# Kernel tuning notes

Hardware: AMD Instinct MI355X
Metric: run time of the kernel (lower is better)

## Reference

```python
import jax, jax.numpy as jnp
import numpy as np

B = 65536          # number of graphs
NPG = 28           # nodes per graph (896 = 32*28)
N = B * NPG
K = 4              # random within-graph neighbors per node


def setup_inputs() -> dict:
    key = jax.random.key(0)
    ks = jax.random.split(key, 8)
    x = jax.random.normal(ks[0], (N, 2), dtype=jnp.float32)
    # within-graph random edges: each node i -> K random targets in its graph
    local = jax.random.randint(ks[1], (N, K), 0, NPG)
    base = (jnp.arange(N, dtype=jnp.int32) // NPG) * NPG
    dst = (base[:, None] + local.astype(jnp.int32)).reshape(-1)
    src = jnp.repeat(jnp.arange(N, dtype=jnp.int32), K)
    edge_index = jnp.stack([src, dst])  # [2, E]
    conv_w = jax.random.normal(ks[2], (2, 32), dtype=jnp.float32) * (1.0 / np.sqrt(2))
    conv_b = jax.random.normal(ks[3], (32,), dtype=jnp.float32) * 0.01
    fc1_w = jax.random.normal(ks[4], (896, 256), dtype=jnp.float32) * (1.0 / np.sqrt(896))
    fc1_b = jax.random.normal(ks[5], (256,), dtype=jnp.float32) * 0.01
    fc2_w = jax.random.normal(ks[6], (256, 2), dtype=jnp.float32) * (1.0 / np.sqrt(256))
    fc2_b = jax.random.normal(ks[7], (2,), dtype=jnp.float32) * 0.01
    return {"x": x, "edge_index": edge_index, "conv_w": conv_w, "conv_b": conv_b,
            "fc1_w": fc1_w, "fc1_b": fc1_b, "fc2_w": fc2_w, "fc2_b": fc2_b}


def gcn_conv(x, edge_index, w, b):
    n = x.shape[0]
    h = x @ w  # [N, 32]
    loops = jnp.arange(n, dtype=edge_index.dtype)
    src = jnp.concatenate([edge_index[0], loops])
    dst = jnp.concatenate([edge_index[1], loops])
    deg = jax.ops.segment_sum(jnp.ones_like(dst, dtype=h.dtype), dst, num_segments=n)
    dinv = jnp.where(deg > 0, jax.lax.rsqrt(jnp.maximum(deg, 1.0)), 0.0)
    norm = dinv[src] * dinv[dst]  # [E']
    agg = jax.ops.segment_sum(h[src] * norm[:, None], dst, num_segments=n)
    return agg + b


def reference(x, edge_index, conv_w, conv_b, fc1_w, fc1_b, fc2_w, fc2_b):
    h = jax.nn.relu(gcn_conv(x, edge_index, conv_w, conv_b))  # [N, 32]
    h = h.reshape(-1, 896)                                    # [B, 896]
    h = h @ fc1_w + fc1_b                                     # [B, 256]
    nrm = jnp.sqrt(jnp.sum(h * h, axis=1, keepdims=True))
    hn = h / jnp.maximum(nrm, 1e-12)                          # F.normalize(dim=1)
    x1 = hn @ fc2_w + fc2_b                                   # [B, 2]
    mu = jax.nn.sigmoid(x1[:, 0])
    theta = jax.nn.softplus(x1[:, 1])
    return hn, mu, theta
```

## Files before the change

### kernel.cpp

```cpp
#include <hip/hip_runtime.h>
#include <hip/hip_bf16.h>
#include <stdint.h>

#define NPG 28
#define KDIM 896
#define NOUT 256
#define BM 128
#define BK 32
#define KT (KDIM / BK)

typedef __attribute__((ext_vector_type(8))) __bf16 bf16x8;
typedef __attribute__((ext_vector_type(8))) ushort us8;
typedef __attribute__((ext_vector_type(4))) float f32x4;

__device__ __forceinline__ ushort f2bf(float v) {
    uint u = __float_as_uint(v);
    return (ushort)((u + 0x7fffu + ((u >> 16) & 1u)) >> 16);
}

__device__ __forceinline__ void gload_lds16(const void* g, void* l) {
    __builtin_amdgcn_global_load_lds(
        (const __attribute__((address_space(1))) void*)(uintptr_t)g,
        (__attribute__((address_space(3))) void*)(uintptr_t)l,
        16, 0, 0);
}

__global__ __launch_bounds__(256) void k_agg(
    const float* __restrict__ x, const int* __restrict__ dst,
    const float* __restrict__ f1w,
    float* __restrict__ acc2g, ushort* __restrict__ wt, int nAgg)
{
    __shared__ int   pk[8][32];
    __shared__ float sx[8][32][2];
    __shared__ float t[32][33];

    const int tid = threadIdx.x;

    if ((int)blockIdx.x >= nAgg) {
        int b = blockIdx.x - nAgg;
        int n0 = (b & 7) * 32, k0 = (b >> 3) * 32;
        int tx = tid & 31, ty = tid >> 5;
#pragma unroll
        for (int q = 0; q < 4; ++q)
            t[ty + q * 8][tx] = f1w[(k0 + ty + q * 8) * NOUT + n0 + tx];
        __syncthreads();
#pragma unroll
        for (int q = 0; q < 4; ++q)
            wt[(long)(k0 >> 5) * (NOUT * BK) + (n0 + ty + q * 8) * BK + tx] =
                f2bf(t[tx][ty + q * 8]);
        return;
    }

    const int g = tid >> 5;
    const int j = tid & 31;
    const long gb = ((long)blockIdx.x * 8 + g) * NPG;

    float2 xx = make_float2(0.f, 0.f);
    if (j < NPG) {
        int4 d4 = ((const int4*)dst)[gb + j];
        xx = ((const float2*)x)[gb + j];
        int gbi = (int)gb;
        pk[g][j] = (d4.x - gbi) | ((d4.y - gbi) << 8) |
                   ((d4.z - gbi) << 16) | ((d4.w - gbi) << 24);
    }
    __syncthreads();

    const uint repj = (uint)j * 0x01010101u;
    uint cp0 = 0, cp1 = 0, cp2 = 0, cp3 = 0;
    int cnt = 0;
#pragma unroll
    for (int s4 = 0; s4 < 7; ++s4) {
        int4 pv = *(const int4*)&pk[g][s4 * 4];
#pragma unroll
        for (int r = 0; r < 4; ++r) {
            uint v = ((const uint*)&pv)[r] ^ repj;
            uint zb = ~(((v & 0x7F7F7F7Fu) + 0x7F7F7F7Fu) | v) & 0x80808080u;
            uint c = (uint)__popc(zb);
            cnt += (int)c;
            int s = s4 * 4 + r;
            uint nib = c << ((s & 7) * 4);
            if (s < 8)       cp0 |= nib;
            else if (s < 16) cp1 |= nib;
            else if (s < 24) cp2 |= nib;
            else             cp3 |= nib;
        }
    }

    const float dinv = rsqrtf((float)(1 + cnt));
    const float sx0 = xx.x * dinv, sx1 = xx.y * dinv;
    if (j < NPG) {
        sx[g][j][0] = sx0;
        sx[g][j][1] = sx1;
    }
    __syncthreads();

    float a0 = sx0, a1 = sx1;
#pragma unroll
    for (int s = 0; s < NPG; ++s) {
        float2 sv = *(const float2*)&sx[g][s][0];
        uint cpw = (s < 8) ? cp0 : (s < 16) ? cp1 : (s < 24) ? cp2 : cp3;
        float cf = (float)((cpw >> ((s & 7) * 4)) & 0xFu);
        a0 += cf * sv.x;
        a1 += cf * sv.y;
    }

    if (j < NPG) {
        const long Btot = (long)nAgg * 8;
        const long graph = (long)blockIdx.x * 8 + g;
        ((float2*)acc2g)[(long)j * Btot + graph] = make_float2(a0 * dinv, a1 * dinv);
    }
}

__device__ __forceinline__ void stage_b2(const char* WtB, ushort* BsX, int kt, int tid) {
    const int o = (tid & 3) ^ ((tid >> 3) & 3);
    const long tb = (long)kt * 16384 + (tid >> 2) * 64 + o * 16;
    gload_lds16(WtB + tb,        (char*)BsX + tid * 16);
    gload_lds16(WtB + tb + 8192, (char*)BsX + 8192 + tid * 16);
}

__device__ __forceinline__ void agen_write(ushort* AsX, float2 av, int awoff,
                                           const float* w0, const float* w1, const float* bb) {
    union { us8 v; uint u[4]; } pk;
#pragma unroll
    for (int k = 0; k < 4; ++k) {
        float e0 = fmaxf(av.x * w0[2 * k]     + av.y * w1[2 * k]     + bb[2 * k],     0.f);
        float e1 = fmaxf(av.x * w0[2 * k + 1] + av.y * w1[2 * k + 1] + bb[2 * k + 1], 0.f);
        __hip_bfloat162 h = __float22bfloat162_rn(make_float2(e0, e1));
        pk.u[k] = *reinterpret_cast<uint*>(&h);
    }
    *(us8*)&AsX[awoff] = pk.v;
}

__device__ __forceinline__ void compute_mfma(const ushort* AsX, const ushort* BsX,
                                             f32x4 acc[4][4], int a_off, int b_off) {
    bf16x8 bfr[4];
#pragma unroll
    for (int ni = 0; ni < 4; ++ni)
        bfr[ni] = *(const bf16x8*)(&BsX[b_off + ni * 512]);
    __builtin_amdgcn_s_setprio(1);
#pragma unroll
    for (int mi = 0; mi < 4; ++mi) {
        bf16x8 af = *(const bf16x8*)(&AsX[a_off + mi * 512]);
#pragma unroll
        for (int ni = 0; ni < 4; ++ni)
            acc[mi][ni] = __builtin_amdgcn_mfma_f32_16x16x32_bf16(
                af, bfr[ni], acc[mi][ni], 0, 0, 0);
    }
    __builtin_amdgcn_s_setprio(0);
}

__global__ __launch_bounds__(512, 4) void k_gemm(
    const float* __restrict__ acc2g, const ushort* __restrict__ Wt,
    const float* __restrict__ cw, const float* __restrict__ cb,
    const float* __restrict__ f1b, const float* __restrict__ f2w,
    const float* __restrict__ f2b, float* __restrict__ out, int Bsz)
{
    __shared__ ushort As0[BM * BK], As1[BM * BK];
    __shared__ ushort Bs0[NOUT * BK], Bs1[NOUT * BK], Bs2[NOUT * BK];
    __shared__ float2 Aring[2][8][64];

    const int tid = threadIdx.x;
    const int w = tid >> 6, l = tid & 63;
    const int wM = w >> 2, wN = w & 3;
    const int l15 = l & 15, lhi = (l >> 4) & 3;
    const long m0 = (long)blockIdx.x * BM;
    const long BszB = (long)Bsz * 8;

    const int ao = __builtin_amdgcn_readfirstlane(w & 3);
    const int arow = (w >> 2) * 64 + l;
    const int awoff = arow * 32 + ((ao ^ ((l >> 1) & 3)) * 8);
    float w0[8], w1[8], bb[8];
#pragma unroll
    for (int k = 0; k < 8; ++k) {
        w0[k] = cw[ao * 8 + k]; w1[k] = cw[32 + ao * 8 + k]; bb[k] = cb[ao * 8 + k];
    }

    const int swz = (lhi ^ ((l15 >> 1) & 3)) * 8;
    const int a_off = (wM * 64 + l15) * 32 + swz;
    const int b_off = (wN * 64 + l15) * 32 + swz;

    const char* A2B = (const char*)acc2g;
    const char* WtB = (const char*)Wt;
    const long agbase = (m0 + (long)(w >> 2) * 64 + 2 * l) * 8;

    f32x4 acc[4][4];
#pragma unroll
    for (int mi = 0; mi < 4; ++mi)
#pragma unroll
        for (int ni = 0; ni < 4; ++ni) acc[mi][ni] = (f32x4){0.f, 0.f, 0.f, 0.f};

    stage_b2(WtB, Bs0, 0, tid);
    if (l < 32) gload_lds16(A2B + agbase,        (char*)&Aring[0][w][0]);
    stage_b2(WtB, Bs1, 1, tid);
    if (l < 32) gload_lds16(A2B + BszB + agbase, (char*)&Aring[1][w][0]);
    asm volatile("s_waitcnt vmcnt(3)" ::: "memory");
    __builtin_amdgcn_s_barrier();
    agen_write(As0, Aring[0][w][l], awoff, w0, w1, bb);
    asm volatile("s_waitcnt lgkmcnt(0)" ::: "memory");
    __builtin_amdgcn_s_barrier();

#define PH(BC, BS, AC, AN, RR, RS, KS) do {                                    \
        stage_b2(WtB, BS, (KS), tid);                                          \
        if (l < 32) gload_lds16(A2B + (long)(KS) * BszB + agbase,              \
                                (char*)&Aring[RS][w][0]);                      \
        compute_mfma(AC, BC, acc, a_off, b_off);                               \
        asm volatile("s_waitcnt vmcnt(3)" ::: "memory");                       \
        agen_write(AN, Aring[RR][w][l], awoff, w0, w1, bb);                    \
        asm volatile("s_waitcnt lgkmcnt(0)" ::: "memory");                     \
        __builtin_amdgcn_s_barrier();                                          \
    } while (0)

    for (int kt = 0; kt < 24; kt += 6) {
        PH(Bs0, Bs2, As0, As1, 1, 0, kt + 2);
        PH(Bs1, Bs0, As1, As0, 0, 1, kt + 3);
        PH(Bs2, Bs1, As0, As1, 1, 0, kt + 4);
        PH(Bs0, Bs2, As1, As0, 0, 1, kt + 5);
        PH(Bs1, Bs0, As0, As1, 1, 0, kt + 6);
        PH(Bs2, Bs1, As1, As0, 0, 1, kt + 7);
    }
    PH(Bs0, Bs2, As0, As1, 1, 0, 26);
    PH(Bs1, Bs0, As1, As0, 0, 1, 27);
    {
        compute_mfma(As0, Bs2, acc, a_off, b_off);
        asm volatile("s_waitcnt vmcnt(0)" ::: "memory");
        agen_write(As1, Aring[1][w][l], awoff, w0, w1, bb);
        asm volatile("s_waitcnt lgkmcnt(0)" ::: "memory");
        __builtin_amdgcn_s_barrier();
    }
    {
        compute_mfma(As1, Bs0, acc, a_off, b_off);
        asm volatile("s_waitcnt lgkmcnt(0)" ::: "memory");
        __builtin_amdgcn_s_barrier();
    }
#undef PH

    float b1[4], w20[4], w21[4];
#pragma unroll
    for (int ni = 0; ni < 4; ++ni) {
        int col = wN * 64 + ni * 16 + l15;
        b1[ni] = f1b[col];
        w20[ni] = f2w[col * 2 + 0];
        w21[ni] = f2w[col * 2 + 1];
    }
    float* red    = (float*)As0;
    float* red_ss = red;
    float* red_p0 = red + 512;
    float* red_p1 = red + 1024;
    float* red_rn = red + 1536;

#pragma unroll
    for (int mi = 0; mi < 4; ++mi) {
        float ssr[4], p0r[4], p1r[4];
#pragma unroll
        for (int r = 0; r < 4; ++r) { ssr[r] = 0.f; p0r[r] = 0.f; p1r[r] = 0.f; }
#pragma unroll
        for (int ni = 0; ni < 4; ++ni) {
#pragma unroll
            for (int r = 0; r < 4; ++r) {
                float v = acc[mi][ni][r] + b1[ni];
                acc[mi][ni][r] = v;
                ssr[r] += v * v;
                p0r[r] += v * w20[ni];
                p1r[r] += v * w21[ni];
            }
        }
#pragma unroll
        for (int m = 1; m < 16; m <<= 1) {
#pragma unroll
            for (int r = 0; r < 4; ++r) {
                ssr[r] += __shfl_xor(ssr[r], m);
                p0r[r] += __shfl_xor(p0r[r], m);
                p1r[r] += __shfl_xor(p1r[r], m);
            }
        }
        if (l15 == 0) {
            int rowb = wM * 64 + mi * 16 + lhi * 4;
#pragma unroll
            for (int r = 0; r < 4; ++r) {
                red_ss[(rowb + r) * 4 + wN] = ssr[r];
                red_p0[(rowb + r) * 4 + wN] = p0r[r];
                red_p1[(rowb + r) * 4 + wN] = p1r[r];
            }
        }
    }
    __syncthreads();

    if (tid < BM) {
        int row = tid;
        float ss = red_ss[row * 4 + 0] + red_ss[row * 4 + 1] + red_ss[row * 4 + 2] + red_ss[row * 4 + 3];
        float p0 = red_p0[row * 4 + 0] + red_p0[row * 4 + 1] + red_p0[row * 4 + 2] + red_p0[row * 4 + 3];
        float p1 = red_p1[row * 4 + 0] + red_p1[row * 4 + 1] + red_p1[row * 4 + 2] + red_p1[row * 4 + 3];
        float rn = 1.0f / fmaxf(sqrtf(ss), 1e-12f);
        float x0 = p0 * rn + f2b[0];
        float x1 = p1 * rn + f2b[1];
        float mu = 1.0f / (1.0f + expf(-x0));
        float th = (x1 > 0.f) ? (x1 + log1pf(expf(-x1))) : log1pf(expf(x1));
        long gr = m0 + row;
        out[(long)Bsz * NOUT + gr] = mu;
        out[(long)Bsz * NOUT + Bsz + gr] = th;
        red_rn[row] = rn;
    }
    __syncthreads();

#pragma unroll
    for (int mi = 0; mi < 4; ++mi) {
        float rn[4];
#pragma unroll
        for (int r = 0; r < 4; ++r) rn[r] = red_rn[wM * 64 + mi * 16 + lhi * 4 + r];
#pragma unroll
        for (int ni = 0; ni < 4; ++ni) {
#pragma unroll
            for (int r = 0; r < 4; ++r) {
                long row = m0 + wM * 64 + mi * 16 + lhi * 4 + r;
                out[row * NOUT + wN * 64 + ni * 16 + l15] = acc[mi][ni][r] * rn[r];
            }
        }
    }
}

extern "C" void kernel_launch(void* const* d_in, const int* in_sizes, int n_in,
                              void* d_out, int out_size, void* d_ws, size_t ws_size,
                              hipStream_t stream) {
    const float* x   = (const float*)d_in[0];
    const int*   ei  = (const int*)d_in[1];
    const float* cw  = (const float*)d_in[2];
    const float* cb  = (const float*)d_in[3];
    const float* f1w = (const float*)d_in[4];
    const float* f1b = (const float*)d_in[5];
    const float* f2w = (const float*)d_in[6];
    const float* f2b = (const float*)d_in[7];
    float* out = (float*)d_out;

    const int Nn  = in_sizes[0] / 2;
    const int Bsz = Nn / NPG;
    const int E   = in_sizes[1] / 2;
    const int* dst = ei + E;

    float*  acc2g = (float*)d_ws;
    ushort* Wt    = (ushort*)(acc2g + (size_t)Nn * 2);

    const int nAgg = Bsz / 8;
    const int nTr  = (KDIM / 32) * (NOUT / 32);

    k_agg<<<nAgg + nTr, 256, 0, stream>>>(x, dst, f1w, acc2g, Wt, nAgg);
    k_gemm<<<Bsz / BM, 512, 0, stream>>>(acc2g, Wt, cw, cb, f1b, f2w, f2b, out, Bsz);
}
```

Baseline: 66.92 us.

## Fuse graph aggregation into GEMM kernel and double M tile

Moves the per-graph degree/aggregation computation into the GEMM kernel, storing aggregated node features in LDS instead of a global workspace, and leaves a small weight-transpose prep kernel. BM grows to 256 with 1024-thread blocks, so each B stage is one load per thread. This removes the global write and readback of the aggregated features. In exchange it needs a large LDS footprint that limits residency to one block per CU, and the aggregation runs serially inside each block before the GEMM starts.

```diff
diff --git a/kernel.cpp b/kernel.cpp
--- a/kernel.cpp
+++ b/kernel.cpp
@@ -5,7 +5,7 @@
 #define NPG 28
 #define KDIM 896
 #define NOUT 256
-#define BM 128
+#define BM 256
 #define BK 32
 #define KT (KDIM / BK)
 
@@ -25,97 +25,28 @@
         16, 0, 0);
 }
 
-__global__ __launch_bounds__(256) void k_agg(
-    const float* __restrict__ x, const int* __restrict__ dst,
-    const float* __restrict__ f1w,
-    float* __restrict__ acc2g, ushort* __restrict__ wt, int nAgg)
+__global__ __launch_bounds__(256) void k_prep(const float* __restrict__ f1w,
+                                              ushort* __restrict__ wt)
 {
-    __shared__ int   pk[8][32];
-    __shared__ float sx[8][32][2];
     __shared__ float t[32][33];
-
     const int tid = threadIdx.x;
-
-    if ((int)blockIdx.x >= nAgg) {
-        int b = blockIdx.x - nAgg;
-        int n0 = (b & 7) * 32, k0 = (b >> 3) * 32;
-        int tx = tid & 31, ty = tid >> 5;
-#pragma unroll
-        for (int q = 0; q < 4; ++q)
-            t[ty + q * 8][tx] = f1w[(k0 + ty + q * 8) * NOUT + n0 + tx];
-        __syncthreads();
-#pragma unroll
-        for (int q = 0; q < 4; ++q)
-            wt[(long)(k0 >> 5) * (NOUT * BK) + (n0 + ty + q * 8) * BK + tx] =
-                f2bf(t[tx][ty + q * 8]);
-        return;
-    }
-
-    const int g = tid >> 5;
-    const int j = tid & 31;
-    const long gb = ((long)blockIdx.x * 8 + g) * NPG;
-
-    float2 xx = make_float2(0.f, 0.f);
-    if (j < NPG) {
-        int4 d4 = ((const int4*)dst)[gb + j];
-        xx = ((const float2*)x)[gb + j];
-        int gbi = (int)gb;
-        pk[g][j] = (d4.x - gbi) | ((d4.y - gbi) << 8) |
-                   ((d4.z - gbi) << 16) | ((d4.w - gbi) << 24);
-    }
+    int b = blockIdx.x;
+    int n0 = (b & 7) * 32, k0 = (b >> 3) * 32;
+    int tx = tid & 31, ty = tid >> 5;
+#pragma unroll
+    for (int q = 0; q < 4; ++q)
+        t[ty + q * 8][tx] = f1w[(k0 + ty + q * 8) * NOUT + n0 + tx];
     __syncthreads();
-
-    const uint repj = (uint)j * 0x01010101u;
-    uint cp0 = 0, cp1 = 0, cp2 = 0, cp3 = 0;
-    int cnt = 0;
-#pragma unroll
-    for (int s4 = 0; s4 < 7; ++s4) {
-        int4 pv = *(const int4*)&pk[g][s4 * 4];
-#pragma unroll
-        for (int r = 0; r < 4; ++r) {
-            uint v = ((const uint*)&pv)[r] ^ repj;
-            uint zb = ~(((v & 0x7F7F7F7Fu) + 0x7F7F7F7Fu) | v) & 0x80808080u;
-            uint c = (uint)__popc(zb);
-            cnt += (int)c;
-            int s = s4 * 4 + r;
-            uint nib = c << ((s & 7) * 4);
-            if (s < 8)       cp0 |= nib;
-            else if (s < 16) cp1 |= nib;
-            else if (s < 24) cp2 |= nib;
-            else             cp3 |= nib;
-        }
-    }
-
-    const float dinv = rsqrtf((float)(1 + cnt));
-    const float sx0 = xx.x * dinv, sx1 = xx.y * dinv;
-    if (j < NPG) {
-        sx[g][j][0] = sx0;
-        sx[g][j][1] = sx1;
-    }
-    __syncthreads();
-
-    float a0 = sx0, a1 = sx1;
-#pragma unroll
-    for (int s = 0; s < NPG; ++s) {
-        float2 sv = *(const float2*)&sx[g][s][0];
-        uint cpw = (s < 8) ? cp0 : (s < 16) ? cp1 : (s < 24) ? cp2 : cp3;
-        float cf = (float)((cpw >> ((s & 7) * 4)) & 0xFu);
-        a0 += cf * sv.x;
-        a1 += cf * sv.y;
-    }
-
-    if (j < NPG) {
-        const long Btot = (long)nAgg * 8;
-        const long graph = (long)blockIdx.x * 8 + g;
-        ((float2*)acc2g)[(long)j * Btot + graph] = make_float2(a0 * dinv, a1 * dinv);
-    }
-}
-
-__device__ __forceinline__ void stage_b2(const char* WtB, ushort* BsX, int kt, int tid) {
+#pragma unroll
+    for (int q = 0; q < 4; ++q)
+        wt[(long)(k0 >> 5) * (NOUT * BK) + (n0 + ty + q * 8) * BK + tx] =
+            f2bf(t[tx][ty + q * 8]);
+}
+
+__device__ __forceinline__ void stage_b1(const char* WtB, ushort* BsX, int kt, int tid) {
     const int o = (tid & 3) ^ ((tid >> 3) & 3);
-    const long tb = (long)kt * 16384 + (tid >> 2) * 64 + o * 16;
-    gload_lds16(WtB + tb,        (char*)BsX + tid * 16);
-    gload_lds16(WtB + tb + 8192, (char*)BsX + 8192 + tid * 16);
+    gload_lds16(WtB + (long)kt * 16384 + (tid >> 2) * 64 + o * 16,
+                (char*)BsX + tid * 16);
 }
 
 __device__ __forceinline__ void agen_write(ushort* AsX, float2 av, int awoff,
@@ -149,22 +80,101 @@
     __builtin_amdgcn_s_setprio(0);
 }
 
-__global__ __launch_bounds__(512, 4) void k_gemm(
-    const float* __restrict__ acc2g, const ushort* __restrict__ Wt,
+__global__ __launch_bounds__(1024, 4) void k_fused(
+    const float* __restrict__ x, const int* __restrict__ dst,
+    const ushort* __restrict__ Wt,
     const float* __restrict__ cw, const float* __restrict__ cb,
     const float* __restrict__ f1b, const float* __restrict__ f2w,
     const float* __restrict__ f2b, float* __restrict__ out, int Bsz)
 {
     __shared__ ushort As0[BM * BK], As1[BM * BK];
     __shared__ ushort Bs0[NOUT * BK], Bs1[NOUT * BK], Bs2[NOUT * BK];
-    __shared__ float2 Aring[2][8][64];
+    __shared__ float2 Agg[NPG][BM];
 
     const int tid = threadIdx.x;
     const int w = tid >> 6, l = tid & 63;
     const int wM = w >> 2, wN = w & 3;
     const int l15 = l & 15, lhi = (l >> 4) & 3;
     const long m0 = (long)blockIdx.x * BM;
-    const long BszB = (long)Bsz * 8;
+    const char* WtB = (const char*)Wt;
+
+    stage_b1(WtB, Bs0, 0, tid);
+    stage_b1(WtB, Bs1, 1, tid);
+
+    {
+        int*   pks = (int*)As0;
+        float* sxp = (float*)As1;
+        const int g5 = tid >> 5;
+        const int j  = tid & 31;
+
+        int4 d4 = make_int4(0, 0, 0, 0);
+        float2 xx = make_float2(0.f, 0.f);
+        {
+            long gb = (m0 + (long)g5 * 8) * NPG;
+            if (j < NPG) {
+                d4 = ((const int4*)dst)[gb + j];
+                xx = ((const float2*)x)[gb + j];
+            }
+        }
+        for (int it = 0; it < 8; ++it) {
+            const int gr = g5 * 8 + it;
+            const long gb = (m0 + gr) * NPG;
+            int4 d4n = make_int4(0, 0, 0, 0);
+            float2 xxn = make_float2(0.f, 0.f);
+            if (it < 7 && j < NPG) {
+                d4n = ((const int4*)dst)[gb + NPG + j];
+                xxn = ((const float2*)x)[gb + NPG + j];
+            }
+            if (j < NPG) {
+                int gbi = (int)gb;
+                pks[g5 * 32 + j] = (d4.x - gbi) | ((d4.y - gbi) << 8) |
+                                   ((d4.z - gbi) << 16) | ((d4.w - gbi) << 24);
+            }
+            asm volatile("s_waitcnt lgkmcnt(0)" ::: "memory");
+
+            const uint repj = (uint)j * 0x01010101u;
+            uint cp0 = 0, cp1 = 0, cp2 = 0, cp3 = 0;
+            int cnt = 0;
+#pragma unroll
+            for (int s4 = 0; s4 < 7; ++s4) {
+                int4 pv = *(const int4*)&pks[g5 * 32 + s4 * 4];
+#pragma unroll
+                for (int r = 0; r < 4; ++r) {
+                    uint v = ((const uint*)&pv)[r] ^ repj;
+                    uint zb = ~(((v & 0x7F7F7F7Fu) + 0x7F7F7F7Fu) | v) & 0x80808080u;
+                    uint c = (uint)__popc(zb);
+                    cnt += (int)c;
+                    int s = s4 * 4 + r;
+                    uint nib = c << ((s & 7) * 4);
+                    if (s < 8)       cp0 |= nib;
+                    else if (s < 16) cp1 |= nib;
+                    else if (s < 24) cp2 |= nib;
+                    else             cp3 |= nib;
+                }
+            }
+
+            const float dinv = rsqrtf((float)(1 + cnt));
+            const float sx0 = xx.x * dinv, sx1 = xx.y * dinv;
+            if (j < NPG) {
+                sxp[(g5 * 32 + j) * 2]     = sx0;
+                sxp[(g5 * 32 + j) * 2 + 1] = sx1;
+            }
+            asm volatile("s_waitcnt lgkmcnt(0)" ::: "memory");
+
+            float a0 = sx0, a1 = sx1;
+#pragma unroll
+            for (int s = 0; s < NPG; ++s) {
+                float2 sv = *(const float2*)&sxp[(g5 * 32 + s) * 2];
+                uint cpw = (s < 8) ? cp0 : (s < 16) ? cp1 : (s < 24) ? cp2 : cp3;
+                float cf = (float)((cpw >> ((s & 7) * 4)) & 0xFu);
+                a0 += cf * sv.x;
+                a1 += cf * sv.y;
+            }
+            if (j < NPG)
+                Agg[j][gr] = make_float2(a0 * dinv, a1 * dinv);
+            d4 = d4n; xx = xxn;
+        }
+    }
 
     const int ao = __builtin_amdgcn_readfirstlane(w & 3);
     const int arow = (w >> 2) * 64 + l;
@@ -174,56 +184,44 @@
     for (int k = 0; k < 8; ++k) {
         w0[k] = cw[ao * 8 + k]; w1[k] = cw[32 + ao * 8 + k]; bb[k] = cb[ao * 8 + k];
     }
-
     const int swz = (lhi ^ ((l15 >> 1) & 3)) * 8;
     const int a_off = (wM * 64 + l15) * 32 + swz;
     const int b_off = (wN * 64 + l15) * 32 + swz;
 
-    const char* A2B = (const char*)acc2g;
-    const char* WtB = (const char*)Wt;
-    const long agbase = (m0 + (long)(w >> 2) * 64 + 2 * l) * 8;
-
     f32x4 acc[4][4];
 #pragma unroll
     for (int mi = 0; mi < 4; ++mi)
 #pragma unroll
         for (int ni = 0; ni < 4; ++ni) acc[mi][ni] = (f32x4){0.f, 0.f, 0.f, 0.f};
 
-    stage_b2(WtB, Bs0, 0, tid);
-    if (l < 32) gload_lds16(A2B + agbase,        (char*)&Aring[0][w][0]);
-    stage_b2(WtB, Bs1, 1, tid);
-    if (l < 32) gload_lds16(A2B + BszB + agbase, (char*)&Aring[1][w][0]);
-    asm volatile("s_waitcnt vmcnt(3)" ::: "memory");
-    __builtin_amdgcn_s_barrier();
-    agen_write(As0, Aring[0][w][l], awoff, w0, w1, bb);
+    __syncthreads();
+    agen_write(As0, Agg[0][arow], awoff, w0, w1, bb);
     asm volatile("s_waitcnt lgkmcnt(0)" ::: "memory");
     __builtin_amdgcn_s_barrier();
 
-#define PH(BC, BS, AC, AN, RR, RS, KS) do {                                    \
-        stage_b2(WtB, BS, (KS), tid);                                          \
-        if (l < 32) gload_lds16(A2B + (long)(KS) * BszB + agbase,              \
-                                (char*)&Aring[RS][w][0]);                      \
+#define PH(BC, BS, AC, AN, KS) do {                                            \
+        stage_b1(WtB, BS, (KS), tid);                                          \
         compute_mfma(AC, BC, acc, a_off, b_off);                               \
-        asm volatile("s_waitcnt vmcnt(3)" ::: "memory");                       \
-        agen_write(AN, Aring[RR][w][l], awoff, w0, w1, bb);                    \
+        asm volatile("s_waitcnt vmcnt(1)" ::: "memory");                       \
+        agen_write(AN, Agg[(KS) - 1][arow], awoff, w0, w1, bb);                \
         asm volatile("s_waitcnt lgkmcnt(0)" ::: "memory");                     \
         __builtin_amdgcn_s_barrier();                                          \
     } while (0)
 
     for (int kt = 0; kt < 24; kt += 6) {
-        PH(Bs0, Bs2, As0, As1, 1, 0, kt + 2);
-        PH(Bs1, Bs0, As1, As0, 0, 1, kt + 3);
-        PH(Bs2, Bs1, As0, As1, 1, 0, kt + 4);
-        PH(Bs0, Bs2, As1, As0, 0, 1, kt + 5);
-        PH(Bs1, Bs0, As0, As1, 1, 0, kt + 6);
-        PH(Bs2, Bs1, As1, As0, 0, 1, kt + 7);
-    }
-    PH(Bs0, Bs2, As0, As1, 1, 0, 26);
-    PH(Bs1, Bs0, As1, As0, 0, 1, 27);
+        PH(Bs0, Bs2, As0, As1, kt + 2);
+        PH(Bs1, Bs0, As1, As0, kt + 3);
+        PH(Bs2, Bs1, As0, As1, kt + 4);
+        PH(Bs0, Bs2, As1, As0, kt + 5);
+        PH(Bs1, Bs0, As0, As1, kt + 6);
+        PH(Bs2, Bs1, As1, As0, kt + 7);
+    }
+    PH(Bs0, Bs2, As0, As1, 26);
+    PH(Bs1, Bs0, As1, As0, 27);
     {
         compute_mfma(As0, Bs2, acc, a_off, b_off);
         asm volatile("s_waitcnt vmcnt(0)" ::: "memory");
-        agen_write(As1, Aring[1][w][l], awoff, w0, w1, bb);
+        agen_write(As1, Agg[27][arow], awoff, w0, w1, bb);
         asm volatile("s_waitcnt lgkmcnt(0)" ::: "memory");
         __builtin_amdgcn_s_barrier();
     }
@@ -244,9 +242,9 @@
     }
     float* red    = (float*)As0;
     float* red_ss = red;
-    float* red_p0 = red + 512;
-    float* red_p1 = red + 1024;
-    float* red_rn = red + 1536;
+    float* red_p0 = red + 1024;
+    float* red_p1 = red + 2048;
+    float* red_rn = red + 3072;
 
 #pragma unroll
     for (int mi = 0; mi < 4; ++mi) {
@@ -336,12 +334,9 @@
     const int E   = in_sizes[1] / 2;
     const int* dst = ei + E;
 
-    float*  acc2g = (float*)d_ws;
-    ushort* Wt    = (ushort*)(acc2g + (size_t)Nn * 2);
-
-    const int nAgg = Bsz / 8;
-    const int nTr  = (KDIM / 32) * (NOUT / 32);
-
-    k_agg<<<nAgg + nTr, 256, 0, stream>>>(x, dst, f1w, acc2g, Wt, nAgg);
-    k_gemm<<<Bsz / BM, 512, 0, stream>>>(acc2g, Wt, cw, cb, f1b, f2w, f2b, out, Bsz);
-}
+    ushort* Wt = (ushort*)d_ws;
+
+    const int nTr = (KDIM / 32) * (NOUT / 32);
+    k_prep<<<nTr, 256, 0, stream>>>(f1w, Wt);
+    k_fused<<<Bsz / BM, 1024, 0, stream>>>(x, dst, Wt, cw, cb, f1b, f2w, f2b, out, Bsz);
+}
```

Result: slower. 73.55 us (+9.9%).
